# Performance work log

Measured on AMD Instinct MI355X. Metric: run time of the kernel, lower is better.

Reference implementation:

```python
import jax, jax.numpy as jnp
import numpy as np

IN1, IN2, OUT = 256, 64, 64

def setup_inputs() -> dict:
    key = jax.random.key(0)
    k1, k2, k3, k4 = jax.random.split(key, 4)
    x1 = jax.random.normal(k1, (4, 4096, IN1), dtype=jnp.float32)
    x2 = jax.random.normal(k2, (4, 4096, IN2), dtype=jnp.float32)
    # nn.Linear(in_1, in_2*out): weight (in_2*out, in_1), bias (in_2*out,)
    W = jax.random.normal(k3, (IN2 * OUT, IN1), dtype=jnp.float32) / np.sqrt(IN1)
    bvec = jax.random.normal(k4, (IN2 * OUT,), dtype=jnp.float32) * 0.01
    return {"x1": x1, "x2": x2, "W": W, "bvec": bvec}

def reference(x1, x2, W, bvec):
    b, n, _ = x1.shape
    # per-token generated weight: (b, n, in_2, out)
    w = (jnp.einsum('bni,oi->bno', x1, W) + bvec).reshape(b, n, IN2, OUT)
    # batched vector-matrix product per token
    y = jnp.einsum('bnj,bnjo->bno', x2, w)
    return y
```

## Files before the change

### kernel.cpp

```cpp
#include <hip/hip_runtime.h>


#define FRAG_SHORTS 512
#define JSTEP (2 * 16 * FRAG_SHORTS)
#define BIAS_OFF ((size_t)(64 * 2 * 16) * FRAG_SHORTS)

typedef __bf16 bf16x8 __attribute__((ext_vector_type(8)));
typedef float  f32x16 __attribute__((ext_vector_type(16)));

static __device__ __forceinline__ unsigned short f2bf(float f) {
  union { float f; unsigned u; } v; v.f = f;
  unsigned r = v.u + 0x7FFFu + ((v.u >> 16) & 1u);
  return (unsigned short)(r >> 16);
}

static __device__ __forceinline__ bf16x8 pack8(float4 a, float4 b) {
  union { bf16x8 v; unsigned short u[8]; } r;
  r.u[0] = f2bf(a.x); r.u[1] = f2bf(a.y); r.u[2] = f2bf(a.z); r.u[3] = f2bf(a.w);
  r.u[4] = f2bf(b.x); r.u[5] = f2bf(b.y); r.u[6] = f2bf(b.z); r.u[7] = f2bf(b.w);
  return r.v;
}

__global__ void prep_w(const float* __restrict__ W, const float* __restrict__ bv,
                       unsigned short* __restrict__ Wf) {
  int idx = blockIdx.x * 256 + threadIdx.x;
  int r  = idx >> 4;
  int ks = idx & 15;
  int j   = r >> 6;
  int o   = r & 63;
  int oh  = o >> 5;
  int l31 = o & 31;
  size_t fb = ((size_t)(j * 2 + oh) * 16 + ks) * FRAG_SHORTS;

  const float4* row = (const float4*)(W + (size_t)r * 256 + ks * 16);
  float4 v0 = row[0], v1 = row[1], v2 = row[2], v3 = row[3];
  ushort4 lo0, lo1, hi0, hi1;
  lo0.x = f2bf(v0.x); lo0.y = f2bf(v0.y); lo0.z = f2bf(v0.z); lo0.w = f2bf(v0.w);
  lo1.x = f2bf(v1.x); lo1.y = f2bf(v1.y); lo1.z = f2bf(v1.z); lo1.w = f2bf(v1.w);
  hi0.x = f2bf(v2.x); hi0.y = f2bf(v2.y); hi0.z = f2bf(v2.z); hi0.w = f2bf(v2.w);
  hi1.x = f2bf(v3.x); hi1.y = f2bf(v3.y); hi1.z = f2bf(v3.z); hi1.w = f2bf(v3.w);
  *(ushort4*)&Wf[fb + l31 * 8 + 0] = lo0;
  *(ushort4*)&Wf[fb + l31 * 8 + 4] = lo1;
  *(ushort4*)&Wf[fb + 256 + l31 * 8 + 0] = hi0;
  *(ushort4*)&Wf[fb + 256 + l31 * 8 + 4] = hi1;

  if (idx < 512) {
    int f   = idx >> 6;
    int ln  = idx & 63;
    int ohb = f >> 2, jq = f & 3;
    int lb  = ln & 31, lgb = ln >> 5;
    #pragma unroll
    for (int e = 0; e < 8; ++e)
      Wf[BIAS_OFF + (size_t)f * FRAG_SHORTS + ln * 8 + e] =
          f2bf(bv[(jq * 16 + 8 * lgb + e) * 64 + 32 * ohb + lb]);
  }
}

__global__
__attribute__((amdgpu_flat_work_group_size(512, 512), amdgpu_waves_per_eu(2, 2)))
void meta_main(const float* __restrict__ x1, const float* __restrict__ x2,
               const unsigned short* __restrict__ Wf, float* __restrict__ out) {
  __shared__ __align__(16) unsigned char smem[102400];
  float* sX2 = (float*)smem;
  float* red = (float*)(smem + 32768);

  const int tid  = threadIdx.x;
  const int lane = tid & 63;
  const int wv   = tid >> 6;
  const int kh   = wv & 3;
  const int jh   = wv >> 2;
  const int l31  = lane & 31;
  const int lg   = lane >> 5;

  const int bid  = blockIdx.x;
  const int oh   = bid & 1;
  const long tile0 = (long)(bid >> 1) * 128;

  {
    const float4* s2 = (const float4*)(x2 + tile0 * 64);
    #pragma unroll
    for (int it = 0; it < 4; ++it) {
      int fi4 = it * 512 + tid;
      float4 v = s2[fi4];
      int token = fi4 >> 4;
      int j0    = (fi4 & 15) * 4;
      sX2[(j0 + 0) * 128 + token] = v.x;
      sX2[(j0 + 1) * 128 + token] = v.y;
      sX2[(j0 + 2) * 128 + token] = v.z;
      sX2[(j0 + 3) * 128 + token] = v.w;
    }
  }

  bf16x8 bf[4][4];
  #pragma unroll
  for (int m = 0; m < 4; ++m) {
    #pragma unroll
    for (int q = 0; q < 4; ++q) {
      const float* p = x1 + (size_t)(tile0 + m * 32 + l31) * 256 +
                       (kh * 4 + q) * 16 + lg * 8;
      bf[m][q] = pack8(*(const float4*)p, *(const float4*)(p + 4));
    }
  }
  __syncthreads();

  f32x16 z;
  #pragma unroll
  for (int r = 0; r < 16; ++r) z[r] = 0.0f;

  f32x16 y[4];
  #pragma unroll
  for (int m = 0; m < 4; ++m) y[m] = z;
  if (kh == 0) {
    #pragma unroll
    for (int qq = 0; qq < 2; ++qq) {
      int jq = jh * 2 + qq;
      bf16x8 bias = *(const bf16x8*)(Wf + BIAS_OFF +
                                     (size_t)(oh * 4 + jq) * FRAG_SHORTS + lane * 8);
      #pragma unroll
      for (int m = 0; m < 4; ++m) {
        union { bf16x8 v; unsigned short u[8]; } xf;
        #pragma unroll
        for (int e = 0; e < 8; ++e)
          xf.u[e] = f2bf(sX2[(jq * 16 + 8 * lg + e) * 128 + m * 32 + l31]);
        y[m] = __builtin_amdgcn_mfma_f32_32x32x16_bf16(bias, xf.v, y[m], 0, 0, 0);
      }
    }
  }

  const unsigned short* wp =
      Wf + ((size_t)(jh * 32 * 2 + oh) * 16 + kh * 4) * FRAG_SHORTS + lane * 8;
  bf16x8 wa[4], wb[4];
  #pragma unroll
  for (int q = 0; q < 4; ++q)
    wa[q] = *(const bf16x8*)(wp + q * FRAG_SHORTS);

#define COMPUTE(WREG, J)                                                        \
  {                                                                             \
    f32x16 aA, aB;                                                              \
    aA = __builtin_amdgcn_mfma_f32_32x32x16_bf16(WREG[0], bf[0][0], z, 0, 0, 0);\
    aB = __builtin_amdgcn_mfma_f32_32x32x16_bf16(WREG[0], bf[1][0], z, 0, 0, 0);\
    aA = __builtin_amdgcn_mfma_f32_32x32x16_bf16(WREG[1], bf[0][1], aA, 0, 0, 0);\
    aB = __builtin_amdgcn_mfma_f32_32x32x16_bf16(WREG[1], bf[1][1], aB, 0, 0, 0);\
    aA = __builtin_amdgcn_mfma_f32_32x32x16_bf16(WREG[2], bf[0][2], aA, 0, 0, 0);\
    aB = __builtin_amdgcn_mfma_f32_32x32x16_bf16(WREG[2], bf[1][2], aB, 0, 0, 0);\
    aA = __builtin_amdgcn_mfma_f32_32x32x16_bf16(WREG[3], bf[0][3], aA, 0, 0, 0);\
    aB = __builtin_amdgcn_mfma_f32_32x32x16_bf16(WREG[3], bf[1][3], aB, 0, 0, 0);\
    float xs0 = sX2[(J) * 128 + l31];                                           \
    float xs1 = sX2[(J) * 128 + 32 + l31];                                      \
    _Pragma("unroll")                                                           \
    for (int r = 0; r < 16; ++r) {                                              \
      y[0][r] += xs0 * aA[r];                                                   \
      y[1][r] += xs1 * aB[r];                                                   \
    }                                                                           \
    aA = __builtin_amdgcn_mfma_f32_32x32x16_bf16(WREG[0], bf[2][0], z, 0, 0, 0);\
    aB = __builtin_amdgcn_mfma_f32_32x32x16_bf16(WREG[0], bf[3][0], z, 0, 0, 0);\
    aA = __builtin_amdgcn_mfma_f32_32x32x16_bf16(WREG[1], bf[2][1], aA, 0, 0, 0);\
    aB = __builtin_amdgcn_mfma_f32_32x32x16_bf16(WREG[1], bf[3][1], aB, 0, 0, 0);\
    aA = __builtin_amdgcn_mfma_f32_32x32x16_bf16(WREG[2], bf[2][2], aA, 0, 0, 0);\
    aB = __builtin_amdgcn_mfma_f32_32x32x16_bf16(WREG[2], bf[3][2], aB, 0, 0, 0);\
    aA = __builtin_amdgcn_mfma_f32_32x32x16_bf16(WREG[3], bf[2][3], aA, 0, 0, 0);\
    aB = __builtin_amdgcn_mfma_f32_32x32x16_bf16(WREG[3], bf[3][3], aB, 0, 0, 0);\
    float xs2 = sX2[(J) * 128 + 64 + l31];                                      \
    float xs3 = sX2[(J) * 128 + 96 + l31];                                      \
    _Pragma("unroll")                                                           \
    for (int r = 0; r < 16; ++r) {                                              \
      y[2][r] += xs2 * aA[r];                                                   \
      y[3][r] += xs3 * aB[r];                                                   \
    }                                                                           \
  }

  for (int i = 0; i < 32; i += 2) {
    const int jg = jh * 32 + i;
    #pragma unroll
    for (int q = 0; q < 4; ++q)
      wb[q] = *(const bf16x8*)(wp + JSTEP + q * FRAG_SHORTS);
    COMPUTE(wa, jg);
    if (i + 2 < 32) {
      #pragma unroll
      for (int q = 0; q < 4; ++q)
        wa[q] = *(const bf16x8*)(wp + 2 * JSTEP + q * FRAG_SHORTS);
    }
    COMPUTE(wb, jg + 1);
    wp += 2 * JSTEP;
  }
#undef COMPUTE

#define RED_W(S)                                                   \
  { float* b = red + (S) * 4352;                                   \
    _Pragma("unroll") for (int m = 0; m < 4; ++m)                  \
      _Pragma("unroll") for (int r = 0; r < 16; ++r)               \
        b[(m * 64 + lane) * 17 + r] = y[m][r]; }
#define RED_A(S)                                                   \
  { const float* b = red + (S) * 4352;                             \
    _Pragma("unroll") for (int m = 0; m < 4; ++m)                  \
      _Pragma("unroll") for (int r = 0; r < 16; ++r)               \
        y[m][r] += b[(m * 64 + lane) * 17 + r]; }

  if (kh >= 2) RED_W((kh - 2) * 2 + jh);
  __syncthreads();
  if (kh < 2)  RED_A(kh * 2 + jh);
  __syncthreads();
  if (kh == 1) RED_W(jh);
  __syncthreads();
  if (kh == 0) RED_A(jh);
  __syncthreads();
  if (kh == 0 && jh == 1) RED_W(0);
  __syncthreads();
  if (wv == 0) {
    RED_A(0);
    #pragma unroll
    for (int m = 0; m < 4; ++m) {
      float* yo = out + (tile0 + m * 32 + l31) * 64 + oh * 32;
      #pragma unroll
      for (int rq = 0; rq < 4; ++rq) {
        float4 v = make_float4(y[m][4 * rq + 0], y[m][4 * rq + 1],
                               y[m][4 * rq + 2], y[m][4 * rq + 3]);
        *(float4*)(yo + 8 * rq + 4 * lg) = v;
      }
    }
  }
#undef RED_W
#undef RED_A
}

extern "C" void kernel_launch(void* const* d_in, const int* in_sizes, int n_in,
                              void* d_out, int out_size, void* d_ws, size_t ws_size,
                              hipStream_t stream) {
  const float* x1 = (const float*)d_in[0];
  const float* x2 = (const float*)d_in[1];
  const float* W  = (const float*)d_in[2];
  const float* bv = (const float*)d_in[3];
  float* y = (float*)d_out;
  unsigned short* Wf = (unsigned short*)d_ws;

  prep_w<<<256, 256, 0, stream>>>(W, bv, Wf);
  meta_main<<<256, 512, 0, stream>>>(x1, x2, Wf, y);
}
```

Baseline: 110.9 us.

## Deepen weight prefetch, stagger j order per block, and prioritize MFMA issue

Replaces the two-buffer weight fragment prefetch with a four-buffer rotation, so three j-steps of weight loads are in flight ahead of the compute. Each block starts its j loop at a different phase derived from its block id, spreading reads of the shared weight buffer across L2/memory channels. It also wraps the MFMA bursts in s_setprio so the matrix work gets issue priority over the FMA accumulation of other waves. The cost is extra VGPRs for the additional buffers, which could cause spills at the forced two waves per EU, plus a few extra wrapped-index loads past the end of the loop.

```diff
diff --git a/kernel.cpp b/kernel.cpp
--- a/kernel.cpp
+++ b/kernel.cpp
@@ -75,6 +75,7 @@
   const int bid  = blockIdx.x;
   const int oh   = bid & 1;
   const long tile0 = (long)(bid >> 1) * 128;
+  const int phase = (bid >> 3) & 31;
 
   {
     const float4* s2 = (const float4*)(x2 + tile0 * 64);
@@ -127,16 +128,24 @@
     }
   }
 
-  const unsigned short* wp =
+  const unsigned short* wbase0 =
       Wf + ((size_t)(jh * 32 * 2 + oh) * 16 + kh * 4) * FRAG_SHORTS + lane * 8;
-  bf16x8 wa[4], wb[4];
-  #pragma unroll
-  for (int q = 0; q < 4; ++q)
-    wa[q] = *(const bf16x8*)(wp + q * FRAG_SHORTS);
-
-#define COMPUTE(WREG, J)                                                        \
+
+#define LOADW(DST, I)                                                           \
   {                                                                             \
+    int jj = ((I) + phase) & 31;                                                \
+    const unsigned short* p = wbase0 + (size_t)jj * JSTEP;                      \
+    DST[0] = *(const bf16x8*)(p + 0 * FRAG_SHORTS);                             \
+    DST[1] = *(const bf16x8*)(p + 1 * FRAG_SHORTS);                             \
+    DST[2] = *(const bf16x8*)(p + 2 * FRAG_SHORTS);                             \
+    DST[3] = *(const bf16x8*)(p + 3 * FRAG_SHORTS);                             \
+  }
+
+#define COMPUTE(WREG, I)                                                        \
+  {                                                                             \
+    const int jg = jh * 32 + (((I) + phase) & 31);                              \
     f32x16 aA, aB;                                                              \
+    __builtin_amdgcn_s_setprio(1);                                              \
     aA = __builtin_amdgcn_mfma_f32_32x32x16_bf16(WREG[0], bf[0][0], z, 0, 0, 0);\
     aB = __builtin_amdgcn_mfma_f32_32x32x16_bf16(WREG[0], bf[1][0], z, 0, 0, 0);\
     aA = __builtin_amdgcn_mfma_f32_32x32x16_bf16(WREG[1], bf[0][1], aA, 0, 0, 0);\
@@ -145,13 +154,15 @@
     aB = __builtin_amdgcn_mfma_f32_32x32x16_bf16(WREG[2], bf[1][2], aB, 0, 0, 0);\
     aA = __builtin_amdgcn_mfma_f32_32x32x16_bf16(WREG[3], bf[0][3], aA, 0, 0, 0);\
     aB = __builtin_amdgcn_mfma_f32_32x32x16_bf16(WREG[3], bf[1][3], aB, 0, 0, 0);\
-    float xs0 = sX2[(J) * 128 + l31];                                           \
-    float xs1 = sX2[(J) * 128 + 32 + l31];                                      \
+    __builtin_amdgcn_s_setprio(0);                                              \
+    float xs0 = sX2[jg * 128 + l31];                                            \
+    float xs1 = sX2[jg * 128 + 32 + l31];                                       \
     _Pragma("unroll")                                                           \
     for (int r = 0; r < 16; ++r) {                                              \
       y[0][r] += xs0 * aA[r];                                                   \
       y[1][r] += xs1 * aB[r];                                                   \
     }                                                                           \
+    __builtin_amdgcn_s_setprio(1);                                              \
     aA = __builtin_amdgcn_mfma_f32_32x32x16_bf16(WREG[0], bf[2][0], z, 0, 0, 0);\
     aB = __builtin_amdgcn_mfma_f32_32x32x16_bf16(WREG[0], bf[3][0], z, 0, 0, 0);\
     aA = __builtin_amdgcn_mfma_f32_32x32x16_bf16(WREG[1], bf[2][1], aA, 0, 0, 0);\
@@ -160,8 +171,9 @@
     aB = __builtin_amdgcn_mfma_f32_32x32x16_bf16(WREG[2], bf[3][2], aB, 0, 0, 0);\
     aA = __builtin_amdgcn_mfma_f32_32x32x16_bf16(WREG[3], bf[2][3], aA, 0, 0, 0);\
     aB = __builtin_amdgcn_mfma_f32_32x32x16_bf16(WREG[3], bf[3][3], aB, 0, 0, 0);\
-    float xs2 = sX2[(J) * 128 + 64 + l31];                                      \
-    float xs3 = sX2[(J) * 128 + 96 + l31];                                      \
+    __builtin_amdgcn_s_setprio(0);                                              \
+    float xs2 = sX2[jg * 128 + 64 + l31];                                       \
+    float xs3 = sX2[jg * 128 + 96 + l31];                                       \
     _Pragma("unroll")                                                           \
     for (int r = 0; r < 16; ++r) {                                              \
       y[2][r] += xs2 * aA[r];                                                   \
@@ -169,21 +181,17 @@
     }                                                                           \
   }
 
-  for (int i = 0; i < 32; i += 2) {
-    const int jg = jh * 32 + i;
-    #pragma unroll
-    for (int q = 0; q < 4; ++q)
-      wb[q] = *(const bf16x8*)(wp + JSTEP + q * FRAG_SHORTS);
-    COMPUTE(wa, jg);
-    if (i + 2 < 32) {
-      #pragma unroll
-      for (int q = 0; q < 4; ++q)
-        wa[q] = *(const bf16x8*)(wp + 2 * JSTEP + q * FRAG_SHORTS);
-    }
-    COMPUTE(wb, jg + 1);
-    wp += 2 * JSTEP;
+  bf16x8 wa[4], wb[4], wc[4], wd[4];
+  LOADW(wa, 0); LOADW(wb, 1); LOADW(wc, 2);
+
+  for (int i = 0; i < 32; i += 4) {
+    LOADW(wd, i + 3); COMPUTE(wa, i);
+    LOADW(wa, i + 4); COMPUTE(wb, i + 1);
+    LOADW(wb, i + 5); COMPUTE(wc, i + 2);
+    LOADW(wc, i + 6); COMPUTE(wd, i + 3);
   }
 #undef COMPUTE
+#undef LOADW
 
 #define RED_W(S)                                                   \
   { float* b = red + (S) * 4352;                                   \
```

New measurement: 381.5 us. 3.44x slower.

## Stream weight fragments through a 4-slot LDS ring with direct global-to-LDS loads

Applied to the files above, without the earlier changes.

Replaces per-wave register double-buffering of the generated-weight fragments with a 4-slot shared-memory ring filled by global_load_lds, staged two iterations ahead with vmcnt waits and a barrier each step. MFMA groups are wrapped in s_setprio to favor matrix issue. This aims to hide global load latency better, but adds a per-iteration block barrier, extra LDS traffic, and raises shared memory to 160KB, which limits occupancy to one block per CU. The ring is reused as the reduction buffer after a final sync.

```diff
diff --git a/kernel.cpp b/kernel.cpp
--- a/kernel.cpp
+++ b/kernel.cpp
@@ -19,6 +19,13 @@
   r.u[0] = f2bf(a.x); r.u[1] = f2bf(a.y); r.u[2] = f2bf(a.z); r.u[3] = f2bf(a.w);
   r.u[4] = f2bf(b.x); r.u[5] = f2bf(b.y); r.u[6] = f2bf(b.z); r.u[7] = f2bf(b.w);
   return r.v;
+}
+
+static __device__ __forceinline__ void gload_lds16(const unsigned short* g,
+                                                   unsigned short* l) {
+  __builtin_amdgcn_global_load_lds(
+      (const __attribute__((address_space(1))) void*)g,
+      (__attribute__((address_space(3))) void*)l, 16, 0, 0);
 }
 
 __global__ void prep_w(const float* __restrict__ W, const float* __restrict__ bv,
@@ -60,8 +67,9 @@
 __attribute__((amdgpu_flat_work_group_size(512, 512), amdgpu_waves_per_eu(2, 2)))
 void meta_main(const float* __restrict__ x1, const float* __restrict__ x2,
                const unsigned short* __restrict__ Wf, float* __restrict__ out) {
-  __shared__ __align__(16) unsigned char smem[102400];
+  __shared__ __align__(16) unsigned char smem[163840];
   float* sX2 = (float*)smem;
+  unsigned short* ringS = (unsigned short*)(smem + 32768);
   float* red = (float*)(smem + 32768);
 
   const int tid  = threadIdx.x;
@@ -126,64 +134,83 @@
       }
     }
   }
-
-  const unsigned short* wp =
-      Wf + ((size_t)(jh * 32 * 2 + oh) * 16 + kh * 4) * FRAG_SHORTS + lane * 8;
-  bf16x8 wa[4], wb[4];
-  #pragma unroll
-  for (int q = 0; q < 4; ++q)
-    wa[q] = *(const bf16x8*)(wp + q * FRAG_SHORTS);
-
-#define COMPUTE(WREG, J)                                                        \
+  __syncthreads();
+
+  const int fragsel = jh * 8192 + (kh * 4) * 512;
+  unsigned short* lds_w = ringS + fragsel;
+  const unsigned short* rd_w = ringS + fragsel + lane * 8;
+  const unsigned short* gsrc0 =
+      Wf + (size_t)jh * 32 * JSTEP + (size_t)(oh * 16 + kh * 4) * FRAG_SHORTS + lane * 8;
+
+#define STAGE(T, SLOT)                                                          \
   {                                                                             \
-    f32x16 aA, aB;                                                              \
-    aA = __builtin_amdgcn_mfma_f32_32x32x16_bf16(WREG[0], bf[0][0], z, 0, 0, 0);\
-    aB = __builtin_amdgcn_mfma_f32_32x32x16_bf16(WREG[0], bf[1][0], z, 0, 0, 0);\
-    aA = __builtin_amdgcn_mfma_f32_32x32x16_bf16(WREG[1], bf[0][1], aA, 0, 0, 0);\
-    aB = __builtin_amdgcn_mfma_f32_32x32x16_bf16(WREG[1], bf[1][1], aB, 0, 0, 0);\
-    aA = __builtin_amdgcn_mfma_f32_32x32x16_bf16(WREG[2], bf[0][2], aA, 0, 0, 0);\
-    aB = __builtin_amdgcn_mfma_f32_32x32x16_bf16(WREG[2], bf[1][2], aB, 0, 0, 0);\
-    aA = __builtin_amdgcn_mfma_f32_32x32x16_bf16(WREG[3], bf[0][3], aA, 0, 0, 0);\
-    aB = __builtin_amdgcn_mfma_f32_32x32x16_bf16(WREG[3], bf[1][3], aB, 0, 0, 0);\
-    float xs0 = sX2[(J) * 128 + l31];                                           \
-    float xs1 = sX2[(J) * 128 + 32 + l31];                                      \
-    _Pragma("unroll")                                                           \
-    for (int r = 0; r < 16; ++r) {                                              \
-      y[0][r] += xs0 * aA[r];                                                   \
-      y[1][r] += xs1 * aB[r];                                                   \
-    }                                                                           \
-    aA = __builtin_amdgcn_mfma_f32_32x32x16_bf16(WREG[0], bf[2][0], z, 0, 0, 0);\
-    aB = __builtin_amdgcn_mfma_f32_32x32x16_bf16(WREG[0], bf[3][0], z, 0, 0, 0);\
-    aA = __builtin_amdgcn_mfma_f32_32x32x16_bf16(WREG[1], bf[2][1], aA, 0, 0, 0);\
-    aB = __builtin_amdgcn_mfma_f32_32x32x16_bf16(WREG[1], bf[3][1], aB, 0, 0, 0);\
-    aA = __builtin_amdgcn_mfma_f32_32x32x16_bf16(WREG[2], bf[2][2], aA, 0, 0, 0);\
-    aB = __builtin_amdgcn_mfma_f32_32x32x16_bf16(WREG[2], bf[3][2], aB, 0, 0, 0);\
-    aA = __builtin_amdgcn_mfma_f32_32x32x16_bf16(WREG[3], bf[2][3], aA, 0, 0, 0);\
-    aB = __builtin_amdgcn_mfma_f32_32x32x16_bf16(WREG[3], bf[3][3], aB, 0, 0, 0);\
-    float xs2 = sX2[(J) * 128 + 64 + l31];                                      \
-    float xs3 = sX2[(J) * 128 + 96 + l31];                                      \
-    _Pragma("unroll")                                                           \
-    for (int r = 0; r < 16; ++r) {                                              \
-      y[2][r] += xs2 * aA[r];                                                   \
-      y[3][r] += xs3 * aB[r];                                                   \
-    }                                                                           \
-  }
-
-  for (int i = 0; i < 32; i += 2) {
-    const int jg = jh * 32 + i;
-    #pragma unroll
-    for (int q = 0; q < 4; ++q)
-      wb[q] = *(const bf16x8*)(wp + JSTEP + q * FRAG_SHORTS);
-    COMPUTE(wa, jg);
-    if (i + 2 < 32) {
-      #pragma unroll
-      for (int q = 0; q < 4; ++q)
-        wa[q] = *(const bf16x8*)(wp + 2 * JSTEP + q * FRAG_SHORTS);
-    }
-    COMPUTE(wb, jg + 1);
-    wp += 2 * JSTEP;
-  }
-#undef COMPUTE
+    const unsigned short* gs = gsrc0 + (size_t)(T) * JSTEP;                     \
+    unsigned short* ls = lds_w + (SLOT) * 16384;                                \
+    gload_lds16(gs + 0 * 512, ls + 0 * 512);                                    \
+    gload_lds16(gs + 1 * 512, ls + 1 * 512);                                    \
+    gload_lds16(gs + 2 * 512, ls + 2 * 512);                                    \
+    gload_lds16(gs + 3 * 512, ls + 3 * 512);                                    \
+  }
+
+  STAGE(0, 0);
+  STAGE(1, 1);
+
+  #pragma unroll 4
+  for (int p = 0; p < 32; ++p) {
+    STAGE((p + 2) & 31, (p + 2) & 3);
+    asm volatile("s_waitcnt vmcnt(8)" ::: "memory");
+    __builtin_amdgcn_s_barrier();
+
+    const unsigned short* rb = rd_w + (p & 3) * 16384;
+    bf16x8 w0 = *(const bf16x8*)(rb + 0 * 512);
+    bf16x8 w1 = *(const bf16x8*)(rb + 1 * 512);
+    bf16x8 w2 = *(const bf16x8*)(rb + 2 * 512);
+    bf16x8 w3 = *(const bf16x8*)(rb + 3 * 512);
+    const int jg = jh * 32 + p;
+
+    f32x16 aA, aB;
+    __builtin_amdgcn_s_setprio(1);
+    aA = __builtin_amdgcn_mfma_f32_32x32x16_bf16(w0, bf[0][0], z, 0, 0, 0);
+    aB = __builtin_amdgcn_mfma_f32_32x32x16_bf16(w0, bf[1][0], z, 0, 0, 0);
+    aA = __builtin_amdgcn_mfma_f32_32x32x16_bf16(w1, bf[0][1], aA, 0, 0, 0);
+    aB = __builtin_amdgcn_mfma_f32_32x32x16_bf16(w1, bf[1][1], aB, 0, 0, 0);
+    aA = __builtin_amdgcn_mfma_f32_32x32x16_bf16(w2, bf[0][2], aA, 0, 0, 0);
+    aB = __builtin_amdgcn_mfma_f32_32x32x16_bf16(w2, bf[1][2], aB, 0, 0, 0);
+    aA = __builtin_amdgcn_mfma_f32_32x32x16_bf16(w3, bf[0][3], aA, 0, 0, 0);
+    aB = __builtin_amdgcn_mfma_f32_32x32x16_bf16(w3, bf[1][3], aB, 0, 0, 0);
+    __builtin_amdgcn_s_setprio(0);
+    {
+      float xs0 = sX2[jg * 128 + l31];
+      float xs1 = sX2[jg * 128 + 32 + l31];
+      #pragma unroll
+      for (int r = 0; r < 16; ++r) {
+        y[0][r] += xs0 * aA[r];
+        y[1][r] += xs1 * aB[r];
+      }
+    }
+    __builtin_amdgcn_s_setprio(1);
+    aA = __builtin_amdgcn_mfma_f32_32x32x16_bf16(w0, bf[2][0], z, 0, 0, 0);
+    aB = __builtin_amdgcn_mfma_f32_32x32x16_bf16(w0, bf[3][0], z, 0, 0, 0);
+    aA = __builtin_amdgcn_mfma_f32_32x32x16_bf16(w1, bf[2][1], aA, 0, 0, 0);
+    aB = __builtin_amdgcn_mfma_f32_32x32x16_bf16(w1, bf[3][1], aB, 0, 0, 0);
+    aA = __builtin_amdgcn_mfma_f32_32x32x16_bf16(w2, bf[2][2], aA, 0, 0, 0);
+    aB = __builtin_amdgcn_mfma_f32_32x32x16_bf16(w2, bf[3][2], aB, 0, 0, 0);
+    aA = __builtin_amdgcn_mfma_f32_32x32x16_bf16(w3, bf[2][3], aA, 0, 0, 0);
+    aB = __builtin_amdgcn_mfma_f32_32x32x16_bf16(w3, bf[3][3], aB, 0, 0, 0);
+    __builtin_amdgcn_s_setprio(0);
+    {
+      float xs2 = sX2[jg * 128 + 64 + l31];
+      float xs3 = sX2[jg * 128 + 96 + l31];
+      #pragma unroll
+      for (int r = 0; r < 16; ++r) {
+        y[2][r] += xs2 * aA[r];
+        y[3][r] += xs3 * aB[r];
+      }
+    }
+  }
+#undef STAGE
+
+  __syncthreads();
 
 #define RED_W(S)                                                   \
   { float* b = red + (S) * 4352;                                   \
```

Result: slower. 113.9 us (+2.7%).
